# Kernel tuning notes

Hardware: AMD Instinct MI355X
Metric: run time of the kernel (lower is better)

## Reference

```python
import jax, jax.numpy as jnp
import numpy as np

B, T, C, H, N = 4, 4096, 2048, 32, 64
DMIX, DDEC = 32, 64
N_LAYER, LAYER_ID = 24, 12
GN_EPS = 1e-5 * 8.0 ** 2  # eps = 1e-5 * head_size_divisor**2


def setup_inputs() -> dict:
    key = jax.random.key(0)
    ks = jax.random.split(key, 24)
    r01 = LAYER_ID / (N_LAYER - 1)
    r1a0 = 1.0 - LAYER_ID / N_LAYER
    ddd = (np.arange(C, dtype=np.float32) / C).reshape(1, 1, C)
    maa = lambda p: jnp.asarray(1.0 - ddd ** p, dtype=jnp.float32)
    # decay speed schedule (canonical RWKV6, over channel dim)
    n = np.arange(C, dtype=np.float32)
    decay = (-6.0 + 5.0 * (n / (C - 1)) ** (0.7 + 1.3 * r01)).reshape(1, 1, C)
    # time_faaaa zigzag schedule
    m = np.arange(C, dtype=np.float32)
    zig = ((m + 1) % 3 - 1) * 0.1
    faaaa = (r01 * (1 - m / (C - 1)) + zig).reshape(H, N)
    s = 1.0 / np.sqrt(C)
    return {
        "x": jax.random.normal(ks[0], (B, T, C), jnp.float32),
        "shift_state": jax.random.normal(ks[1], (B, C), jnp.float32),
        "wkv_state": jnp.zeros((B, H, N, N), jnp.float32),
        "time_maa_x": maa(r1a0),
        "time_maa_w": maa(r1a0),
        "time_maa_k": maa(r1a0),
        "time_maa_v": jnp.asarray(1.0 - (ddd ** r1a0 + 0.3 * r01), jnp.float32),
        "time_maa_r": maa(0.5 * r1a0),
        "time_maa_g": maa(0.5 * r1a0),
        "time_maa_w1": jax.random.normal(ks[2], (C, 5 * DMIX), jnp.float32) * 0.01,
        "time_maa_w2": jax.random.uniform(ks[3], (5, DMIX, C), jnp.float32, -0.01, 0.01),
        "time_decay": jnp.asarray(decay, jnp.float32),
        "time_decay_w1": jax.random.normal(ks[4], (C, DDEC), jnp.float32) * 0.01,
        "time_decay_w2": jax.random.uniform(ks[5], (DDEC, C), jnp.float32, -0.01, 0.01),
        "time_faaaa": jnp.asarray(faaaa, jnp.float32),
        "Wr": jax.random.normal(ks[6], (C, C), jnp.float32) * s,
        "Wk": jax.random.normal(ks[7], (C, C), jnp.float32) * s,
        "Wv": jax.random.normal(ks[8], (C, C), jnp.float32) * s,
        "Wg": jax.random.normal(ks[9], (C, C), jnp.float32) * s,
        "Wo": jax.random.normal(ks[10], (C, C), jnp.float32) * s,
        "gn_weight": jnp.ones((C,), jnp.float32),
        "gn_bias": jnp.zeros((C,), jnp.float32),
    }


def reference(x, shift_state, wkv_state, time_maa_x, time_maa_w, time_maa_k,
              time_maa_v, time_maa_r, time_maa_g, time_maa_w1, time_maa_w2,
              time_decay, time_decay_w1, time_decay_w2, time_faaaa,
              Wr, Wk, Wv, Wg, Wo, gn_weight, gn_bias):
    b, t, c = x.shape
    # token shift: previous token (seeded by shift_state) minus current
    xx = jnp.concatenate([shift_state[:, None, :], x[:, :-1]], axis=1) - x
    lx = x[:, -1]
    # LoRA token-shift mixing
    xxx = x + xx * time_maa_x
    t5 = jnp.tanh(xxx @ time_maa_w1).reshape(b, t, 5, DMIX)
    mixes = jnp.einsum('btfd,fdc->fbtc', t5, time_maa_w2)
    mw, mk, mv, mr, mg = mixes
    xw = x + xx * (time_maa_w + mw)
    xk = x + xx * (time_maa_k + mk)
    xv = x + xx * (time_maa_v + mv)
    xr = x + xx * (time_maa_r + mr)
    xg = x + xx * (time_maa_g + mg)
    r = xr @ Wr
    k = xk @ Wk
    v = xv @ Wv
    g = jax.nn.silu(xg @ Wg)
    # data-dependent decay via LoRA; wkv6 uses log-decay -exp(w)
    w = time_decay + jnp.tanh(xw @ time_decay_w1) @ time_decay_w2
    glog = -jnp.exp(w)  # [b,t,c]
    to_heads = lambda z: z.reshape(b, t, H, N).transpose(1, 0, 2, 3)  # [t,b,h,n]
    rh, kh, vh, gh = to_heads(r), to_heads(k), to_heads(v), to_heads(glog)
    u = time_faaaa  # [H,N]

    def step(S, inp):
        r_t, k_t, v_t, g_t = inp  # each [b,h,n]
        kv = jnp.einsum('bhk,bhv->bhkv', k_t, v_t)
        o_t = jnp.einsum('bhk,bhkv->bhv', r_t, S + u[None, :, :, None] * kv)
        S = jnp.exp(g_t)[..., None] * S + kv
        return S, o_t

    state, o = jax.lax.scan(step, wkv_state, (rh, kh, vh, gh))
    o = o.transpose(1, 0, 2, 3).reshape(b, t, c)  # [b,t,c]
    # GroupNorm with H groups over channel dim
    og = o.reshape(b, t, H, N)
    mu = og.mean(-1, keepdims=True)
    var = og.var(-1, keepdims=True)
    on = (og - mu) * jax.lax.rsqrt(var + GN_EPS)
    on = on * gn_weight.reshape(H, N) + gn_bias.reshape(H, N)
    out = (on.reshape(b, t, c) * g) @ Wo
    return out, lx, state
```

## Files before the change

kernel.cpp:

```cpp
#include <hip/hip_runtime.h>
#include <hip/hip_bf16.h>
#include <stdint.h>

#define DEV __device__ __forceinline__

typedef __bf16 bf16x8 __attribute__((ext_vector_type(8)));
typedef float f32x4 __attribute__((ext_vector_type(4)));
typedef unsigned short u16x8 __attribute__((ext_vector_type(8)));

constexpr int kB = 4, kT = 4096, kC = 2048, kH = 32, kN = 64;
constexpr int kM = kB * kT;
constexpr int SEGN = 8, TSEG = kT / SEGN, CHN = TSEG / 64;

DEV float bfu2f(unsigned short u) {
  union { uint32_t i; float f; } x; x.i = ((uint32_t)u) << 16; return x.f;
}
DEV unsigned short f2bfu(float f) {
  union { float f; uint32_t i; } x; x.f = f;
  uint32_t r = x.i + 0x7FFFu + ((x.i >> 16) & 1u);
  return (unsigned short)(r >> 16);
}

DEV void gld16(const void* g, void* l) {
  __builtin_amdgcn_global_load_lds(
      (const __attribute__((address_space(1))) void*)g,
      (__attribute__((address_space(3))) void*)l, 16, 0, 0);
}

DEV int swzb(int row, int byteoff) { return (row << 7) + (byteoff ^ ((row & 7) << 4)); }
DEV int swz64(int row, int byteoff) { return (row << 6) + (byteoff ^ ((row & 3) << 4)); }

__global__ __launch_bounds__(256) void trans_bf16(
    const float* __restrict__ in, unsigned short* __restrict__ out, int R, int Cn) {
  __shared__ __attribute__((aligned(16))) unsigned short tile[64][65];
  const int t = threadIdx.x;
  const int r0 = blockIdx.y * 64, c0 = blockIdx.x * 64;
  const int lr = t >> 6, lc = t & 63;
#pragma unroll
  for (int i = 0; i < 16; i++) {
    int rr = lr + i * 4;
    int gr = r0 + rr, gc = c0 + lc;
    if (gr < R && gc < Cn) tile[rr][lc] = f2bfu(in[(size_t)gr * Cn + gc]);
  }
  __syncthreads();
#pragma unroll
  for (int i = 0; i < 16; i++) {
    int cc = lr + i * 4;
    int gc = c0 + cc, gr = r0 + lc;
    if (gc < Cn && gr < R) out[(size_t)gc * R + gr] = tile[lc][cc];
  }
}

__global__ __launch_bounds__(256) void prep_x2(
    const float* __restrict__ x, const float* __restrict__ shift,
    const float* __restrict__ maax,
    unsigned short* __restrict__ xxx, float* __restrict__ lx) {
  size_t i4 = ((size_t)blockIdx.x * 256 + threadIdx.x) * 4;
  int c = (int)(i4 & (kC - 1));
  size_t bt = i4 >> 11;
  int tt = (int)(bt & (kT - 1));
  int b = (int)(bt >> 12);
  float4 xv = *(const float4*)(x + i4);
  float4 pv = (tt == 0) ? *(const float4*)(shift + (size_t)b * kC + c)
                        : *(const float4*)(x + i4 - kC);
  float4 mx = *(const float4*)(maax + c);
  ushort4 o4;
  o4.x = f2bfu(xv.x + (pv.x - xv.x) * mx.x);
  o4.y = f2bfu(xv.y + (pv.y - xv.y) * mx.y);
  o4.z = f2bfu(xv.z + (pv.z - xv.z) * mx.z);
  o4.w = f2bfu(xv.w + (pv.w - xv.w) * mx.w);
  *(ushort4*)(xxx + i4) = o4;
  if (tt == kT - 1) *(float4*)(lx + (size_t)b * kC + c) = xv;
}

enum { E_F32 = 0, E_BF16 = 1, E_TANH = 2, E_SILU = 3 };

template <int BM, int BN, int EPI>
__global__ __launch_bounds__(256) void gemm_k(
    const unsigned short* __restrict__ A, const unsigned short* __restrict__ Bt,
    void* __restrict__ Cout, int M, int N, int K) {
  constexpr int WGM = (BM == 128 && BN == 128) ? 2 : (BM == 64 ? 2 : 4);
  constexpr int WGN = 4 / WGM;
  constexpr int WM = BM / WGM, WN = BN / WGN;
  constexpr int WR = WM / 16, WC = WN / 16;
  __shared__ __attribute__((aligned(16))) unsigned short As[BM * 32];
  __shared__ __attribute__((aligned(16))) unsigned short Bs[BN * 32];
  const int t = threadIdx.x, wid = t >> 6, l = t & 63;
  const int m0 = blockIdx.x * BM, n0 = blockIdx.y * BN;
  const int wm0 = (wid / WGN) * WM, wn0 = (wid % WGN) * WN;
  f32x4 acc[WR][WC];
#pragma unroll
  for (int i = 0; i < WR; i++)
#pragma unroll
    for (int j = 0; j < WC; j++) acc[i][j] = f32x4{0.f, 0.f, 0.f, 0.f};

  const int rowS = t >> 2, cbS = (t & 3) * 16;
  const char* Ab = (const char*)A;
  const char* Bb = (const char*)Bt;
  const int aoff = (wm0 + (l & 15)) * 32 + (l >> 4) * 8;
  const int boff = (wn0 + (l & 15)) * 32 + (l >> 4) * 8;

  for (int kt = 0; kt < K; kt += 32) {
#pragma unroll
    for (int ia = 0; ia < BM / 64; ia++)
      gld16(Ab + ((size_t)(m0 + ia * 64 + rowS) * K + kt) * 2 + cbS,
            (char*)As + ia * 4096 + wid * 1024);
    if constexpr (BN >= 64) {
#pragma unroll
      for (int ib = 0; ib < BN / 64; ib++)
        gld16(Bb + ((size_t)(n0 + ib * 64 + rowS) * K + kt) * 2 + cbS,
              (char*)Bs + ib * 4096 + wid * 1024);
    } else {
      if (t < BN * 4)
        gld16(Bb + ((size_t)(n0 + rowS) * K + kt) * 2 + cbS,
              (char*)Bs + wid * 1024);
    }
    __syncthreads();
    bf16x8 af[WR], bfv[WC];
#pragma unroll
    for (int mi = 0; mi < WR; mi++) af[mi] = *(const bf16x8*)(&As[aoff + mi * 512]);
#pragma unroll
    for (int ni = 0; ni < WC; ni++) bfv[ni] = *(const bf16x8*)(&Bs[boff + ni * 512]);
#pragma unroll
    for (int mi = 0; mi < WR; mi++)
#pragma unroll
      for (int ni = 0; ni < WC; ni++)
        acc[mi][ni] = __builtin_amdgcn_mfma_f32_16x16x32_bf16(af[mi], bfv[ni], acc[mi][ni], 0, 0, 0);
    __syncthreads();
  }

#pragma unroll
  for (int mi = 0; mi < WR; mi++) {
#pragma unroll
    for (int ni = 0; ni < WC; ni++) {
      int row = m0 + wm0 + mi * 16 + (l >> 4) * 4;
      int col = n0 + wn0 + ni * 16 + (l & 15);
#pragma unroll
      for (int j = 0; j < 4; j++) {
        float v = acc[mi][ni][j];
        size_t idx = (size_t)(row + j) * N + col;
        if constexpr (EPI == E_F32) ((float*)Cout)[idx] = v;
        else if constexpr (EPI == E_BF16) ((unsigned short*)Cout)[idx] = f2bfu(v);
        else if constexpr (EPI == E_TANH) ((unsigned short*)Cout)[idx] = f2bfu(tanhf(v));
        else if constexpr (EPI == E_SILU) ((unsigned short*)Cout)[idx] = f2bfu(v / (1.f + expf(-v)));
      }
    }
  }
}

template <int EPI>
__global__ __launch_bounds__(512, 2) void gemm256_k(
    const unsigned short* __restrict__ A, const unsigned short* __restrict__ Bt,
    void* __restrict__ Cout, int M, int N, int K) {
  extern __shared__ __attribute__((aligned(16))) char lds[];
  const int tid = threadIdx.x, wid = tid >> 6, l = tid & 63;
  const int fr = l & 15, fq = l >> 4;

  const int mtiles = M >> 8, ntiles = N >> 8;
  const int slab = mtiles >> 3;
  const int xcd = blockIdx.x & 7, loc = blockIdx.x >> 3;
  const int m0 = (xcd * slab + loc / ntiles) * 256;
  const int n0 = (loc % ntiles) * 256;

  const int wm = (wid >> 2) * 128, wn = (wid & 3) * 64;

  const int srow0 = tid >> 2;
  const int scb = ((tid & 3) * 16) ^ ((srow0 & 3) << 4);
  const char* pa2[2]; const char* pb2[2];
#pragma unroll
  for (int i = 0; i < 2; i++) {
    pa2[i] = (const char*)A + (size_t)(m0 + i * 128 + srow0) * K * 2 + scb;
    pb2[i] = (const char*)Bt + (size_t)(n0 + i * 128 + srow0) * K * 2 + scb;
  }

  const char* vA[8]; const char* vB[4];
#pragma unroll
  for (int mi = 0; mi < 8; mi++)
    vA[mi] = lds + swz64(wm + mi * 16 + fr, fq * 16);
#pragma unroll
  for (int ni = 0; ni < 4; ni++)
    vB[ni] = lds + 32768 + swz64(wn + ni * 16 + fr, fq * 16);

  f32x4 acc[8][4];
#pragma unroll
  for (int i = 0; i < 8; i++)
#pragma unroll
    for (int j = 0; j < 4; j++) acc[i][j] = f32x4{0.f, 0.f, 0.f, 0.f};

  auto STG = [&](int q, int s, int ktb) {
    const int d = q * 65536 + s * 16384 + wid * 1024;
    gld16(pa2[0] + ktb + s * 64, lds + d);
    gld16(pa2[1] + ktb + s * 64, lds + d + 8192);
    gld16(pb2[0] + ktb + s * 64, lds + 32768 + d);
    gld16(pb2[1] + ktb + s * 64, lds + 32768 + d + 8192);
  };

  auto PH = [&](int p, int s, bool doStage, int ktbNext, int vm) {
    if (vm)
      asm volatile("s_waitcnt vmcnt(4)" ::: "memory");
    else
      asm volatile("s_waitcnt vmcnt(0)" ::: "memory");
    __builtin_amdgcn_s_barrier();
    __builtin_amdgcn_sched_barrier(0);
    const int pb = p * 65536 + s * 16384;
    bf16x8 a[8], b[4];
#pragma unroll
    for (int mi = 0; mi < 8; mi++) a[mi] = *(const bf16x8*)(vA[mi] + pb);
#pragma unroll
    for (int ni = 0; ni < 4; ni++) b[ni] = *(const bf16x8*)(vB[ni] + pb);
    if (doStage) STG(p ^ 1, s, ktbNext);
    __builtin_amdgcn_sched_barrier(0);
    __builtin_amdgcn_s_setprio(1);
#pragma unroll
    for (int ni = 0; ni < 4; ni++)
#pragma unroll
      for (int mi = 0; mi < 8; mi++)
        acc[mi][ni] = __builtin_amdgcn_mfma_f32_16x16x32_bf16(a[mi], b[ni], acc[mi][ni], 0, 0, 0);
    __builtin_amdgcn_s_setprio(0);
  };

  const int KT = K >> 6;
  STG(0, 0, 0);
  STG(0, 1, 0);

  int T = 0;
  for (; T + 2 < KT; T += 2) {
    PH(0, 0, true, (T + 1) * 128, 4);
    PH(0, 1, true, (T + 1) * 128, 4);
    PH(1, 0, true, (T + 2) * 128, 4);
    PH(1, 1, true, (T + 2) * 128, 4);
  }
  PH(0, 0, true, (KT - 1) * 128, 4);
  PH(0, 1, true, (KT - 1) * 128, 4);
  PH(1, 0, false, 0, 4);
  PH(1, 1, false, 0, 0);

#pragma unroll
  for (int mi = 0; mi < 8; mi++)
#pragma unroll
    for (int ni = 0; ni < 4; ni++) {
      int row = m0 + wm + mi * 16 + fq * 4;
      int col = n0 + wn + ni * 16 + fr;
#pragma unroll
      for (int j = 0; j < 4; j++) {
        float v = acc[mi][ni][j];
        size_t idx = (size_t)(row + j) * N + col;
        if constexpr (EPI == E_F32) ((float*)Cout)[idx] = v;
        else if constexpr (EPI == E_BF16) ((unsigned short*)Cout)[idx] = f2bfu(v);
        else if constexpr (EPI == E_SILU) ((unsigned short*)Cout)[idx] = f2bfu(v / (1.f + expf(-v)));
      }
    }
}

__global__ __launch_bounds__(256) void mix5f_k(
    const unsigned short* __restrict__ t5, const unsigned short* __restrict__ w2t,
    const float* __restrict__ x, const float* __restrict__ shift,
    const float* __restrict__ maaw, const float* __restrict__ maak,
    const float* __restrict__ maav, const float* __restrict__ maar,
    const float* __restrict__ maag,
    unsigned short* __restrict__ xw, unsigned short* __restrict__ xk,
    unsigned short* __restrict__ xvo, unsigned short* __restrict__ xr,
    unsigned short* __restrict__ xg) {
  __shared__ __attribute__((aligned(16))) float tile[64][68];
  const int t = threadIdx.x, wid = t >> 6, l = t & 63;
  const int m0 = blockIdx.x * 64, n0 = blockIdx.y * 64;
  const int wm0 = (wid >> 1) * 32, wn0 = (wid & 1) * 32;
  const int fr = l & 15, fq = l >> 4;

  const unsigned short* pa0 = t5 + (size_t)(m0 + wm0 + fr) * 160 + fq * 8;
  const unsigned short* pa1 = t5 + (size_t)(m0 + wm0 + 16 + fr) * 160 + fq * 8;
  const unsigned short* pb0 = w2t + (size_t)(n0 + wn0 + fr) * 160 + fq * 8;
  const unsigned short* pb1 = w2t + (size_t)(n0 + wn0 + 16 + fr) * 160 + fq * 8;

  const int rrow = m0 + (t >> 2);
  const int c0 = (t & 3) * 16;
  const size_t base = (size_t)rrow * kC + n0 + c0;
  float xreg[16], dreg[16];
  {
    const int tt = rrow & (kT - 1);
    const float* pvp = (tt == 0) ? (shift + (size_t)(rrow >> 12) * kC + n0 + c0)
                                 : (x + base - kC);
#pragma unroll
    for (int q = 0; q < 4; q++) {
      float4 xv4 = *(const float4*)(x + base + q * 4);
      float4 pv4 = *(const float4*)(pvp + q * 4);
      xreg[q * 4 + 0] = xv4.x; dreg[q * 4 + 0] = pv4.x - xv4.x;
      xreg[q * 4 + 1] = xv4.y; dreg[q * 4 + 1] = pv4.y - xv4.y;
      xreg[q * 4 + 2] = xv4.z; dreg[q * 4 + 2] = pv4.z - xv4.z;
      xreg[q * 4 + 3] = xv4.w; dreg[q * 4 + 3] = pv4.w - xv4.w;
    }
  }

  unsigned short* outs[5] = { xw, xk, xvo, xr, xg };
  const float* maas[5] = { maaw, maak, maav, maar, maag };
#pragma unroll
  for (int f = 0; f < 5; f++) {
    bf16x8 a0 = *(const bf16x8*)(pa0 + f * 32);
    bf16x8 a1 = *(const bf16x8*)(pa1 + f * 32);
    bf16x8 b0 = *(const bf16x8*)(pb0 + f * 32);
    bf16x8 b1 = *(const bf16x8*)(pb1 + f * 32);
    f32x4 ac00 = __builtin_amdgcn_mfma_f32_16x16x32_bf16(a0, b0, f32x4{0.f, 0.f, 0.f, 0.f}, 0, 0, 0);
    f32x4 ac01 = __builtin_amdgcn_mfma_f32_16x16x32_bf16(a0, b1, f32x4{0.f, 0.f, 0.f, 0.f}, 0, 0, 0);
    f32x4 ac10 = __builtin_amdgcn_mfma_f32_16x16x32_bf16(a1, b0, f32x4{0.f, 0.f, 0.f, 0.f}, 0, 0, 0);
    f32x4 ac11 = __builtin_amdgcn_mfma_f32_16x16x32_bf16(a1, b1, f32x4{0.f, 0.f, 0.f, 0.f}, 0, 0, 0);
    __syncthreads();
#pragma unroll
    for (int j = 0; j < 4; j++) {
      tile[wm0 + fq * 4 + j][wn0 + fr]            = ac00[j];
      tile[wm0 + fq * 4 + j][wn0 + 16 + fr]       = ac01[j];
      tile[wm0 + 16 + fq * 4 + j][wn0 + fr]       = ac10[j];
      tile[wm0 + 16 + fq * 4 + j][wn0 + 16 + fr]  = ac11[j];
    }
    __syncthreads();
    const float* mp = maas[f] + n0 + c0;
    u16x8 o0, o1;
#pragma unroll
    for (int q = 0; q < 4; q++) {
      f32x4 m4 = *(const f32x4*)&tile[t >> 2][c0 + q * 4];
      float4 ma4 = *(const float4*)(mp + q * 4);
      float mv[4] = { ma4.x, ma4.y, ma4.z, ma4.w };
#pragma unroll
      for (int e = 0; e < 4; e++) {
        int i = q * 4 + e;
        unsigned short r = f2bfu(xreg[i] + dreg[i] * (mv[e] + m4[e]));
        if (i < 8) o0[i] = r; else o1[i - 8] = r;
      }
    }
    *(u16x8*)(outs[f] + base) = o0;
    *(u16x8*)(outs[f] + base + 8) = o1;
  }
}

__global__ __launch_bounds__(256) void wkv_local_k(
    const unsigned short* __restrict__ kb, const unsigned short* __restrict__ vb,
    const unsigned short* __restrict__ dtmp, const unsigned short* __restrict__ td2t,
    const float* __restrict__ tdec,
    float* __restrict__ Lbuf, float* __restrict__ Dseg) {
  const int bid = blockIdx.x;
  const int bh = bid >> 3, seg = bid & 7;
  const int h = bh & 31, b = bh >> 5;
  const int tid = threadIdx.x, w = tid >> 6, l = tid & 63;
  __shared__ __attribute__((aligned(16))) char arena[32768];
  char* KQks = arena;
  char* Vt   = arena + 8192;
  float* EdB = (float*)arena;
  char* TdB  = arena + 16384;
  char* DtA  = arena + 24576;
  __shared__ float segp[4][64];
  __shared__ float DLs[64];
  __shared__ float tdf[64];

  const int fr = l & 15, fq = l >> 4;
  f32x4 Sreg[4];
#pragma unroll
  for (int ni = 0; ni < 4; ni++) Sreg[ni] = f32x4{0.f, 0.f, 0.f, 0.f};

  {
    int r1 = tid >> 3, r2 = 32 + r1;
    int cb1 = ((tid & 7) * 16) ^ ((r1 & 7) << 4);
    int cb2 = ((tid & 7) * 16) ^ ((r2 & 7) << 4);
    gld16((const char*)td2t + (size_t)(h * 64 + r1) * 128 + cb1, TdB + w * 1024);
    gld16((const char*)td2t + (size_t)(h * 64 + r2) * 128 + cb2, TdB + 4096 + w * 1024);
    if (tid < 64) tdf[tid] = tdec[h * 64 + tid];
  }

  float dtot = 1.f;
  float kv[16], vv[16];
  {
    size_t g = ((size_t)b * kT + seg * TSEG + w * 16) * kC + h * 64 + l;
#pragma unroll
    for (int i = 0; i < 16; i++) {
      kv[i] = bfu2f(kb[g]); vv[i] = bfu2f(vb[g]);
      g += kC;
    }
  }

  for (int ch = 0; ch < CHN; ++ch) {
    const size_t gt0 = (size_t)b * kT + seg * TSEG + ch * 64;
    {
      int r1 = tid >> 3, r2 = 32 + r1;
      int cb1 = ((tid & 7) * 16) ^ ((r1 & 7) << 4);
      int cb2 = ((tid & 7) * 16) ^ ((r2 & 7) << 4);
      gld16((const char*)dtmp + (gt0 + r1) * 128 + cb1, DtA + w * 1024);
      gld16((const char*)dtmp + (gt0 + r2) * 128 + cb2, DtA + 4096 + w * 1024);
    }
    __syncthreads();

    f32x4 dacc[4];
    {
      bf16x8 af0 = *(const bf16x8*)(DtA + swzb(w * 16 + fr, fq * 16));
      bf16x8 af1 = *(const bf16x8*)(DtA + swzb(w * 16 + fr, fq * 16 + 64));
#pragma unroll
      for (int nj = 0; nj < 4; nj++) {
        bf16x8 b0 = *(const bf16x8*)(TdB + swzb(nj * 16 + fr, fq * 16));
        bf16x8 b1 = *(const bf16x8*)(TdB + swzb(nj * 16 + fr, fq * 16 + 64));
        dacc[nj] = __builtin_amdgcn_mfma_f32_16x16x32_bf16(af0, b0, f32x4{0.f, 0.f, 0.f, 0.f}, 0, 0, 0);
        dacc[nj] = __builtin_amdgcn_mfma_f32_16x16x32_bf16(af1, b1, dacc[nj], 0, 0, 0);
      }
    }
#pragma unroll
    for (int nj = 0; nj < 4; nj++) {
      float tv = tdf[nj * 16 + fr];
#pragma unroll
      for (int j = 0; j < 4; j++)
        EdB[(w * 16 + fq * 4 + j) * 64 + nj * 16 + fr] = expf(-expf(dacc[nj][j] + tv));
    }
    float dvv[16];
    float p = 1.f;
#pragma unroll
    for (int i = 0; i < 16; i++) {
      float d = EdB[(w * 16 + i) * 64 + l];
      dvv[i] = d; p *= d;
    }
    segp[w][l] = p;
    __syncthreads();

    float pre = 1.f;
    if (w > 0) pre *= segp[0][l];
    if (w > 1) pre *= segp[1][l];
    if (w > 2) pre *= segp[2][l];
    if (w == 3) DLs[l] = pre * p;

    unsigned short kqrow[16], vtrow[16];
    float run = pre;
#pragma unroll
    for (int i = 0; i < 16; i++) {
      run *= dvv[i];
      kqrow[i] = f2bfu(kv[i] / run);
      vtrow[i] = f2bfu(vv[i]);
    }
    {
      u16x8 q0, q1, v0, v1;
#pragma unroll
      for (int j = 0; j < 8; j++) { q0[j] = kqrow[j]; q1[j] = kqrow[j + 8]; v0[j] = vtrow[j]; v1[j] = vtrow[j + 8]; }
      *(u16x8*)(KQks + swzb(l, w * 32)) = q0;
      *(u16x8*)(KQks + swzb(l, w * 32 + 16)) = q1;
      *(u16x8*)(Vt + swzb(l, w * 32)) = v0;
      *(u16x8*)(Vt + swzb(l, w * 32 + 16)) = v1;
    }
    if (ch < CHN - 1) {
      size_t g = ((size_t)b * kT + seg * TSEG + (ch + 1) * 64 + w * 16) * kC + h * 64 + l;
#pragma unroll
      for (int i = 0; i < 16; i++) {
        kv[i] = bfu2f(kb[g]); vv[i] = bfu2f(vb[g]);
        g += kC;
      }
    }
    __syncthreads();

    bf16x8 kA0 = *(const bf16x8*)(KQks + swzb(w * 16 + fr, fq * 16));
    bf16x8 kA1 = *(const bf16x8*)(KQks + swzb(w * 16 + fr, fq * 16 + 64));
    f32x4 kvacc[4];
#pragma unroll
    for (int ni = 0; ni < 4; ni++) {
      bf16x8 bv0 = *(const bf16x8*)(Vt + swzb(ni * 16 + fr, fq * 16));
      bf16x8 bv1 = *(const bf16x8*)(Vt + swzb(ni * 16 + fr, fq * 16 + 64));
      kvacc[ni] = __builtin_amdgcn_mfma_f32_16x16x32_bf16(kA0, bv0, f32x4{0.f, 0.f, 0.f, 0.f}, 0, 0, 0);
      kvacc[ni] = __builtin_amdgcn_mfma_f32_16x16x32_bf16(kA1, bv1, kvacc[ni], 0, 0, 0);
    }
    float dlj[4];
#pragma unroll
    for (int j = 0; j < 4; j++) dlj[j] = DLs[w * 16 + fq * 4 + j];
#pragma unroll
    for (int ni = 0; ni < 4; ni++)
#pragma unroll
      for (int j = 0; j < 4; j++)
        Sreg[ni][j] = (Sreg[ni][j] + kvacc[ni][j]) * dlj[j];
    dtot *= DLs[l];
  }

  float* Lp = Lbuf + (size_t)bid * 4096;
#pragma unroll
  for (int ni = 0; ni < 4; ni++)
#pragma unroll
    for (int j = 0; j < 4; j++)
      Lp[(size_t)(w * 16 + fq * 4 + j) * 64 + ni * 16 + fr] = Sreg[ni][j];
  if (w == 0) Dseg[(size_t)bid * 64 + l] = dtot;
}

__global__ __launch_bounds__(256) void wkv_combine_k(
    const float* __restrict__ s0, const float* __restrict__ Dseg,
    float* __restrict__ Lbuf, float* __restrict__ sOut) {
  const int bh = blockIdx.x, tid = threadIdx.x;
  const int k = tid >> 2, v0 = (tid & 3) * 16;
  float4 s[4];
  const float* sp = s0 + (size_t)bh * 4096 + (size_t)k * 64 + v0;
#pragma unroll
  for (int q = 0; q < 4; q++) s[q] = ((const float4*)sp)[q];
  for (int seg = 0; seg < SEGN; ++seg) {
    size_t idx = (size_t)bh * SEGN + seg;
    float d = Dseg[idx * 64 + k];
    float* Lp = Lbuf + idx * 4096 + (size_t)k * 64 + v0;
#pragma unroll
    for (int q = 0; q < 4; q++) {
      float4 lq = ((float4*)Lp)[q];
      ((float4*)Lp)[q] = s[q];
      s[q].x = d * s[q].x + lq.x; s[q].y = d * s[q].y + lq.y;
      s[q].z = d * s[q].z + lq.z; s[q].w = d * s[q].w + lq.w;
    }
  }
  float* op = sOut + (size_t)bh * 4096 + (size_t)k * 64 + v0;
#pragma unroll
  for (int q = 0; q < 4; q++) ((float4*)op)[q] = s[q];
}

__global__ __launch_bounds__(256) void wkv_seg_k(
    const unsigned short* __restrict__ rb, const unsigned short* __restrict__ kb,
    const unsigned short* __restrict__ vb,
    const unsigned short* __restrict__ dtmp, const unsigned short* __restrict__ td2t,
    const float* __restrict__ tdec,
    const float* __restrict__ uf, const float* __restrict__ Sini,
    unsigned short* __restrict__ o) {
  const int bid = blockIdx.x;
  const int bh = bid >> 3, seg = bid & 7;
  const int h = bh & 31, b = bh >> 5;
  const int tid = threadIdx.x, w = tid >> 6, l = tid & 63;
  __shared__ __attribute__((aligned(16))) char arena[65536];
  char* RQ   = arena;
  char* KQsk = arena + 8192;
  char* KQks = arena + 16384;
  char* Vt   = arena + 24576;
  char* Pl   = arena + 32768;
  char* S0T  = arena + 40960;
  char* RU   = arena + 49152;
  char* Ksk  = arena + 57344;
  float* EdB = (float*)arena;
  char* DtA  = RU;
  char* TdB  = Ksk;
  __shared__ float segp[4][64];
  __shared__ float DLs[64];
  __shared__ float tdf[64];

  const float uu = uf[h * 64 + l];
  const int fr = l & 15, fq = l >> 4;
  if (tid < 64) tdf[tid] = tdec[h * 64 + tid];

  f32x4 Sreg[4];
#pragma unroll
  for (int ni = 0; ni < 4; ni++)
#pragma unroll
    for (int j = 0; j < 4; j++) {
      int kk2 = w * 16 + fq * 4 + j, vv2 = ni * 16 + fr;
      float sv = Sini[(size_t)bid * 4096 + (size_t)kk2 * 64 + vv2];
      Sreg[ni][j] = sv;
      *(unsigned short*)(S0T + swzb(vv2, kk2 * 2)) = f2bfu(sv);
    }
  __syncthreads();

  float rv[16], kv[16], vv[16];
  {
    size_t g = ((size_t)b * kT + seg * TSEG + w * 16) * kC + h * 64 + l;
#pragma unroll
    for (int i = 0; i < 16; i++) {
      rv[i] = bfu2f(rb[g]); kv[i] = bfu2f(kb[g]); vv[i] = bfu2f(vb[g]);
      g += kC;
    }
  }

  const int r1s = tid >> 3, r2s = 32 + r1s;
  const int cb1 = ((tid & 7) * 16) ^ ((r1s & 7) << 4);
  const int cb2 = ((tid & 7) * 16) ^ ((r2s & 7) << 4);

  for (int ch = 0; ch < CHN; ++ch) {
    const size_t gt0 = (size_t)b * kT + seg * TSEG + ch * 64;
    gld16((const char*)dtmp + (gt0 + r1s) * 128 + cb1, DtA + w * 1024);
    gld16((const char*)dtmp + (gt0 + r2s) * 128 + cb2, DtA + 4096 + w * 1024);
    gld16((const char*)td2t + (size_t)(h * 64 + r1s) * 128 + cb1, TdB + w * 1024);
    gld16((const char*)td2t + (size_t)(h * 64 + r2s) * 128 + cb2, TdB + 4096 + w * 1024);
    __syncthreads();

    f32x4 dacc[4];
    {
      bf16x8 af0 = *(const bf16x8*)(DtA + swzb(w * 16 + fr, fq * 16));
      bf16x8 af1 = *(const bf16x8*)(DtA + swzb(w * 16 + fr, fq * 16 + 64));
#pragma unroll
      for (int nj = 0; nj < 4; nj++) {
        bf16x8 b0 = *(const bf16x8*)(TdB + swzb(nj * 16 + fr, fq * 16));
        bf16x8 b1 = *(const bf16x8*)(TdB + swzb(nj * 16 + fr, fq * 16 + 64));
        dacc[nj] = __builtin_amdgcn_mfma_f32_16x16x32_bf16(af0, b0, f32x4{0.f, 0.f, 0.f, 0.f}, 0, 0, 0);
        dacc[nj] = __builtin_amdgcn_mfma_f32_16x16x32_bf16(af1, b1, dacc[nj], 0, 0, 0);
      }
    }
#pragma unroll
    for (int nj = 0; nj < 4; nj++) {
      float tv = tdf[nj * 16 + fr];
#pragma unroll
      for (int j = 0; j < 4; j++)
        EdB[(w * 16 + fq * 4 + j) * 64 + nj * 16 + fr] = expf(-expf(dacc[nj][j] + tv));
    }
    float dv[16];
    float p = 1.f;
#pragma unroll
    for (int i = 0; i < 16; i++) {
      dv[i] = EdB[(w * 16 + i) * 64 + l];
      p *= dv[i];
    }
    segp[w][l] = p;
    __syncthreads();

    float pre = 1.f;
    if (w > 0) pre *= segp[0][l];
    if (w > 1) pre *= segp[1][l];
    if (w > 2) pre *= segp[2][l];
    if (w == 3) DLs[l] = pre * p;

    unsigned short kqrow[16], vtrow[16];
    float run = pre;
#pragma unroll
    for (int i = 0; i < 16; i++) {
      int t = w * 16 + i;
      float rq = rv[i] * run;
      run *= dv[i];
      float kq = kv[i] / run;
      *(unsigned short*)(RQ + swzb(t, l * 2)) = f2bfu(rq);
      *(unsigned short*)(RU + swzb(t, l * 2)) = f2bfu(rv[i] * uu);
      *(unsigned short*)(Ksk + swzb(t, l * 2)) = f2bfu(kv[i]);
      unsigned short kqu = f2bfu(kq);
      *(unsigned short*)(KQsk + swzb(t, l * 2)) = kqu;
      kqrow[i] = kqu;
      vtrow[i] = f2bfu(vv[i]);
    }
    {
      u16x8 q0, q1, v0, v1;
#pragma unroll
      for (int j = 0; j < 8; j++) { q0[j] = kqrow[j]; q1[j] = kqrow[j + 8]; v0[j] = vtrow[j]; v1[j] = vtrow[j + 8]; }
      *(u16x8*)(KQks + swzb(l, w * 32)) = q0;
      *(u16x8*)(KQks + swzb(l, w * 32 + 16)) = q1;
      *(u16x8*)(Vt + swzb(l, w * 32)) = v0;
      *(u16x8*)(Vt + swzb(l, w * 32 + 16)) = v1;
    }

    if (ch < CHN - 1) {
      size_t g = ((size_t)b * kT + seg * TSEG + (ch + 1) * 64 + w * 16) * kC + h * 64 + l;
#pragma unroll
      for (int i = 0; i < 16; i++) {
        rv[i] = bfu2f(rb[g]); kv[i] = bfu2f(kb[g]); vv[i] = bfu2f(vb[g]);
        g += kC;
      }
    }
    __syncthreads();

    bf16x8 a0 = *(const bf16x8*)(RQ + swzb(w * 16 + fr, fq * 16));
    bf16x8 a1 = *(const bf16x8*)(RQ + swzb(w * 16 + fr, fq * 16 + 64));
    f32x4 pacc[4];
#pragma unroll
    for (int ni = 0; ni < 4; ni++) {
      bf16x8 b0 = *(const bf16x8*)(KQsk + swzb(ni * 16 + fr, fq * 16));
      bf16x8 b1 = *(const bf16x8*)(KQsk + swzb(ni * 16 + fr, fq * 16 + 64));
      pacc[ni] = __builtin_amdgcn_mfma_f32_16x16x32_bf16(a0, b0, f32x4{0.f, 0.f, 0.f, 0.f}, 0, 0, 0);
      pacc[ni] = __builtin_amdgcn_mfma_f32_16x16x32_bf16(a1, b1, pacc[ni], 0, 0, 0);
    }
    f32x4 dacc2;
    {
      bf16x8 ru0 = *(const bf16x8*)(RU + swzb(w * 16 + fr, fq * 16));
      bf16x8 ru1 = *(const bf16x8*)(RU + swzb(w * 16 + fr, fq * 16 + 64));
      bf16x8 kb0 = *(const bf16x8*)(Ksk + swzb(w * 16 + fr, fq * 16));
      bf16x8 kb1 = *(const bf16x8*)(Ksk + swzb(w * 16 + fr, fq * 16 + 64));
      dacc2 = __builtin_amdgcn_mfma_f32_16x16x32_bf16(ru0, kb0, f32x4{0.f, 0.f, 0.f, 0.f}, 0, 0, 0);
      dacc2 = __builtin_amdgcn_mfma_f32_16x16x32_bf16(ru1, kb1, dacc2, 0, 0, 0);
    }
    float dg[4];
#pragma unroll
    for (int j = 0; j < 4; j++) dg[j] = __shfl(dacc2[j], fq * 20 + j, 64);
#pragma unroll
    for (int ni = 0; ni < 4; ni++)
#pragma unroll
      for (int j = 0; j < 4; j++) {
        int row = w * 16 + fq * 4 + j, col = ni * 16 + fr;
        float pv = pacc[ni][j];
        pv = (col < row) ? pv : ((col == row) ? dg[j] : 0.f);
        *(unsigned short*)(Pl + swzb(row, col * 2)) = f2bfu(pv);
      }
    __syncthreads();

    bf16x8 pA0 = *(const bf16x8*)(Pl + swzb(w * 16 + fr, fq * 16));
    bf16x8 pA1 = *(const bf16x8*)(Pl + swzb(w * 16 + fr, fq * 16 + 64));
    bf16x8 kA0 = *(const bf16x8*)(KQks + swzb(w * 16 + fr, fq * 16));
    bf16x8 kA1 = *(const bf16x8*)(KQks + swzb(w * 16 + fr, fq * 16 + 64));
    f32x4 oacc[4], kvacc[4];
#pragma unroll
    for (int ni = 0; ni < 4; ni++) {
      bf16x8 bv0 = *(const bf16x8*)(Vt + swzb(ni * 16 + fr, fq * 16));
      bf16x8 bv1 = *(const bf16x8*)(Vt + swzb(ni * 16 + fr, fq * 16 + 64));
      bf16x8 bs0 = *(const bf16x8*)(S0T + swzb(ni * 16 + fr, fq * 16));
      bf16x8 bs1 = *(const bf16x8*)(S0T + swzb(ni * 16 + fr, fq * 16 + 64));
      oacc[ni] = __builtin_amdgcn_mfma_f32_16x16x32_bf16(pA0, bv0, f32x4{0.f, 0.f, 0.f, 0.f}, 0, 0, 0);
      oacc[ni] = __builtin_amdgcn_mfma_f32_16x16x32_bf16(pA1, bv1, oacc[ni], 0, 0, 0);
      oacc[ni] = __builtin_amdgcn_mfma_f32_16x16x32_bf16(a0, bs0, oacc[ni], 0, 0, 0);
      oacc[ni] = __builtin_amdgcn_mfma_f32_16x16x32_bf16(a1, bs1, oacc[ni], 0, 0, 0);
      kvacc[ni] = __builtin_amdgcn_mfma_f32_16x16x32_bf16(kA0, bv0, f32x4{0.f, 0.f, 0.f, 0.f}, 0, 0, 0);
      kvacc[ni] = __builtin_amdgcn_mfma_f32_16x16x32_bf16(kA1, bv1, kvacc[ni], 0, 0, 0);
    }
    size_t obase = gt0 * kC + h * 64;
#pragma unroll
    for (int ni = 0; ni < 4; ni++)
#pragma unroll
      for (int j = 0; j < 4; j++)
        o[obase + (size_t)(w * 16 + fq * 4 + j) * kC + ni * 16 + fr] = f2bfu(oacc[ni][j]);
    __syncthreads();

    float dlj[4];
#pragma unroll
    for (int j = 0; j < 4; j++) dlj[j] = DLs[w * 16 + fq * 4 + j];
#pragma unroll
    for (int ni = 0; ni < 4; ni++)
#pragma unroll
      for (int j = 0; j < 4; j++) {
        int kk2 = w * 16 + fq * 4 + j, vv2 = ni * 16 + fr;
        float sn = (Sreg[ni][j] + kvacc[ni][j]) * dlj[j];
        Sreg[ni][j] = sn;
        *(unsigned short*)(S0T + swzb(vv2, kk2 * 2)) = f2bfu(sn);
      }
  }
}

__global__ __launch_bounds__(256) void gn_k(
    const unsigned short* __restrict__ o, const unsigned short* __restrict__ gb,
    const float* __restrict__ gnw, const float* __restrict__ gnb,
    unsigned short* __restrict__ y) {
  int gi = blockIdx.x * 4 + (threadIdx.x >> 6);
  int j = threadIdx.x & 63;
  int bt = gi >> 5, h = gi & 31;
  size_t idx = (size_t)bt * kC + h * 64 + j;
  float val = bfu2f(o[idx]);
  float s = val, s2 = val * val;
#pragma unroll
  for (int m = 1; m < 64; m <<= 1) {
    s += __shfl_xor(s, m, 64);
    s2 += __shfl_xor(s2, m, 64);
  }
  float mu = s * 0.015625f;
  float var = s2 * 0.015625f - mu * mu;
  float rs = rsqrtf(var + 6.4e-4f);
  float on = (val - mu) * rs * gnw[h * 64 + j] + gnb[h * 64 + j];
  y[idx] = f2bfu(on * bfu2f(gb[idx]));
}

constexpr size_t SZW     = (size_t)2048 * 2048 * 2;
constexpr size_t OFF_WRT = 0;
constexpr size_t OFF_WKT = 1 * SZW;
constexpr size_t OFF_WVT = 2 * SZW;
constexpr size_t OFF_WGT = 3 * SZW;
constexpr size_t OFF_WOT = 4 * SZW;
constexpr size_t OFF_W1T = 5 * SZW;
constexpr size_t OFF_W2T = OFF_W1T + (size_t)160 * 2048 * 2;
constexpr size_t OFF_TD1 = OFF_W2T + (size_t)2048 * 160 * 2;
constexpr size_t OFF_TD2 = OFF_TD1 + (size_t)64 * 2048 * 2;
constexpr size_t OFF_T5  = OFF_TD2 + (size_t)2048 * 64 * 2;
constexpr size_t OFF_DT  = OFF_T5 + (size_t)kM * 160 * 2;
constexpr size_t OFF_XG  = OFF_DT + (size_t)kM * 64 * 2;
constexpr size_t OFF_X   = OFF_XG + (size_t)kM * kC * 4;
constexpr size_t OFF_R   = OFF_X + (size_t)kM * kC * 2;
constexpr size_t OFF_K   = OFF_R + (size_t)kM * kC * 2;
constexpr size_t OFF_V   = OFF_K + (size_t)kM * kC * 2;
constexpr size_t OFF_L   = OFF_WRT;

extern "C" void kernel_launch(void* const* d_in, const int* in_sizes, int n_in,
                              void* d_out, int out_size, void* d_ws, size_t ws_size,
                              hipStream_t stream) {
  const float* x     = (const float*)d_in[0];
  const float* shift = (const float*)d_in[1];
  const float* s0    = (const float*)d_in[2];
  const float* maax  = (const float*)d_in[3];
  const float* maaw  = (const float*)d_in[4];
  const float* maak  = (const float*)d_in[5];
  const float* maav  = (const float*)d_in[6];
  const float* maar  = (const float*)d_in[7];
  const float* maag  = (const float*)d_in[8];
  const float* w1    = (const float*)d_in[9];
  const float* w2    = (const float*)d_in[10];
  const float* tdec  = (const float*)d_in[11];
  const float* tdw1  = (const float*)d_in[12];
  const float* tdw2  = (const float*)d_in[13];
  const float* faaaa = (const float*)d_in[14];
  const float* Wr    = (const float*)d_in[15];
  const float* Wk    = (const float*)d_in[16];
  const float* Wv    = (const float*)d_in[17];
  const float* Wg    = (const float*)d_in[18];
  const float* Wo    = (const float*)d_in[19];
  const float* gnw   = (const float*)d_in[20];
  const float* gnb   = (const float*)d_in[21];

  char* ws = (char*)d_ws;
  unsigned short* Wrt  = (unsigned short*)(ws + OFF_WRT);
  unsigned short* Wkt  = (unsigned short*)(ws + OFF_WKT);
  unsigned short* Wvt  = (unsigned short*)(ws + OFF_WVT);
  unsigned short* Wgt  = (unsigned short*)(ws + OFF_WGT);
  unsigned short* Wot  = (unsigned short*)(ws + OFF_WOT);
  unsigned short* w1t  = (unsigned short*)(ws + OFF_W1T);
  unsigned short* w2t  = (unsigned short*)(ws + OFF_W2T);
  unsigned short* td1t = (unsigned short*)(ws + OFF_TD1);
  unsigned short* td2t = (unsigned short*)(ws + OFF_TD2);
  unsigned short* t5   = (unsigned short*)(ws + OFF_T5);
  unsigned short* dtmp = (unsigned short*)(ws + OFF_DT);
  unsigned short* xg   = (unsigned short*)(ws + OFF_XG);
  unsigned short* obuf = (unsigned short*)(ws + OFF_XG);
  unsigned short* ybuf = (unsigned short*)(ws + OFF_XG) + (size_t)kM * kC;
  unsigned short* bufX = (unsigned short*)(ws + OFF_X);
  unsigned short* bufR = (unsigned short*)(ws + OFF_R);
  unsigned short* bufK = (unsigned short*)(ws + OFF_K);
  unsigned short* bufV = (unsigned short*)(ws + OFF_V);
  float*          Lbuf = (float*)(ws + OFF_L);
  float*          DsegP= (float*)(ws + OFF_TD1);

  float* outp  = (float*)d_out;
  float* lx    = outp + (size_t)kM * kC;
  float* stOut = lx + (size_t)kB * kC;

  dim3 blk(256);

  trans_bf16<<<dim3(32, 32), blk, 0, stream>>>(Wr, Wrt, 2048, 2048);
  trans_bf16<<<dim3(32, 32), blk, 0, stream>>>(Wk, Wkt, 2048, 2048);
  trans_bf16<<<dim3(32, 32), blk, 0, stream>>>(Wv, Wvt, 2048, 2048);
  trans_bf16<<<dim3(32, 32), blk, 0, stream>>>(Wg, Wgt, 2048, 2048);
  trans_bf16<<<dim3(32, 32), blk, 0, stream>>>(Wo, Wot, 2048, 2048);
  trans_bf16<<<dim3(3, 32), blk, 0, stream>>>(w1, w1t, 2048, 160);
  trans_bf16<<<dim3(1, 32), blk, 0, stream>>>(tdw1, td1t, 2048, 64);
  trans_bf16<<<dim3(32, 1), blk, 0, stream>>>(tdw2, td2t, 64, 2048);
  trans_bf16<<<dim3(32, 3), blk, 0, stream>>>(w2, w2t, 160, 2048);

  prep_x2<<<dim3(kM * kC / 4 / 256), blk, 0, stream>>>(x, shift, maax, bufX, lx);

  gemm_k<128, 32, E_TANH><<<dim3(kM / 128, 5), blk, 0, stream>>>(bufX, w1t, t5, kM, 160, 2048);

  dim3 mgrid(kM / 64, kC / 64);
  constexpr int G256 = (kM / 256) * (kC / 256);
  constexpr size_t LDS256 = 131072;

  mix5f_k<<<mgrid, blk, 0, stream>>>(t5, w2t, x, shift, maaw, maak, maav, maar, maag,
                                     bufX, bufV, bufR, bufK, xg);
  gemm_k<64, 64, E_TANH><<<dim3(kM / 64, 1), blk, 0, stream>>>(bufX, td1t, dtmp, kM, 64, 2048);

  gemm256_k<E_BF16><<<dim3(G256), dim3(512), LDS256, stream>>>(bufV, Wkt, bufX, kM, 2048, 2048);
  gemm256_k<E_BF16><<<dim3(G256), dim3(512), LDS256, stream>>>(bufR, Wvt, bufV, kM, 2048, 2048);
  gemm256_k<E_BF16><<<dim3(G256), dim3(512), LDS256, stream>>>(bufK, Wrt, bufR, kM, 2048, 2048);
  gemm256_k<E_SILU><<<dim3(G256), dim3(512), LDS256, stream>>>(xg, Wgt, bufK, kM, 2048, 2048);

  wkv_local_k<<<dim3(kB * kH * SEGN), blk, 0, stream>>>(bufX, bufV, dtmp, td2t, tdec,
                                                        Lbuf, DsegP);
  wkv_combine_k<<<dim3(kB * kH), blk, 0, stream>>>(s0, DsegP, Lbuf, stOut);
  wkv_seg_k<<<dim3(kB * kH * SEGN), blk, 0, stream>>>(bufR, bufX, bufV, dtmp, td2t, tdec,
                                                      faaaa, Lbuf, obuf);

  gn_k<<<dim3(kM * kH / 4), blk, 0, stream>>>(obuf, bufK, gnw, gnb, ybuf);

  gemm256_k<E_F32><<<dim3(G256), dim3(512), LDS256, stream>>>(ybuf, Wot, outp, kM, 2048, 2048);
}
```

Before: 1.436 ms.

## Restructure 256x256 GEMM main loop into 4-phase ping-pong with 128B swizzle

Rewrites the bf16 256x256-tile GEMM mainloop to use full 64-wide K tiles with a 128-byte XOR swizzle. Each K tile is split into four phases: each phase loads A fragments for two M subtiles, and B fragments are reused across phases. Global-to-LDS staging of the next tile is split between phases 0 and 1 (A then B). Barriers bracket each MFMA cluster, launch bounds drop to one block per CU, and a single vmcnt(0) wait per tile replaces the old per-phase waits. The aim is better overlap of LDS reads with MFMA and fewer redundant LDS loads, at the cost of more barriers and lower occupancy.

```diff
diff --git a/kernel.cpp b/kernel.cpp
--- a/kernel.cpp
+++ b/kernel.cpp
@@ -28,7 +28,6 @@
 }
 
 DEV int swzb(int row, int byteoff) { return (row << 7) + (byteoff ^ ((row & 7) << 4)); }
-DEV int swz64(int row, int byteoff) { return (row << 6) + (byteoff ^ ((row & 3) << 4)); }
 
 __global__ __launch_bounds__(256) void trans_bf16(
     const float* __restrict__ in, unsigned short* __restrict__ out, int R, int Cn) {
@@ -148,13 +147,63 @@
   }
 }
 
+#define GPH(PP, QQ, SKIND, KTB)                                                        \
+  do {                                                                                 \
+    const int aB_ = (PP) * 65536 + wr * 16384;                                         \
+    const int bB_ = 32768 + (PP) * 65536 + bh * 16384;                                 \
+    if ((QQ) == 0) {                                                                   \
+      _Pragma("unroll")                                                                \
+      for (int ni = 0; ni < 4; ni++) {                                                 \
+        bfr[ni][0] = *(const bf16x8*)(lds + bB_ + bRow[ni] + bOffK0);                  \
+        bfr[ni][1] = *(const bf16x8*)(lds + bB_ + bRow[ni] + bOffK1);                  \
+      }                                                                                \
+    }                                                                                  \
+    bf16x8 a0k0_ = *(const bf16x8*)(lds + aB_ + (2 * (QQ)) * 2048 + aOffK0);           \
+    bf16x8 a0k1_ = *(const bf16x8*)(lds + aB_ + (2 * (QQ)) * 2048 + aOffK1);           \
+    bf16x8 a1k0_ = *(const bf16x8*)(lds + aB_ + (2 * (QQ) + 1) * 2048 + aOffK0);       \
+    bf16x8 a1k1_ = *(const bf16x8*)(lds + aB_ + (2 * (QQ) + 1) * 2048 + aOffK1);       \
+    if ((SKIND) == 1) {                                                                \
+      const int d_ = ((PP) ^ 1) * 65536;                                               \
+      gld16(pA0 + (KTB), lds + d_ + tid * 16);                                         \
+      gld16(pA0 + (KTB) + (size_t)64 * kC * 2, lds + d_ + 8192 + tid * 16);            \
+      gld16(pA1 + (KTB), lds + d_ + 16384 + tid * 16);                                 \
+      gld16(pA1 + (KTB) + (size_t)64 * kC * 2, lds + d_ + 24576 + tid * 16);           \
+    } else if ((SKIND) == 2) {                                                         \
+      const int d_ = 32768 + (((PP) ^ 1) * 65536);                                     \
+      gld16(pB0 + (KTB), lds + d_ + tid * 16);                                         \
+      gld16(pB0 + (KTB) + (size_t)64 * kC * 2, lds + d_ + 8192 + tid * 16);            \
+      gld16(pB1 + (KTB), lds + d_ + 16384 + tid * 16);                                 \
+      gld16(pB1 + (KTB) + (size_t)64 * kC * 2, lds + d_ + 24576 + tid * 16);           \
+    }                                                                                  \
+    __builtin_amdgcn_s_barrier();                                                      \
+    asm volatile("s_waitcnt lgkmcnt(0)" ::: "memory");                                 \
+    __builtin_amdgcn_sched_barrier(0);                                                 \
+    __builtin_amdgcn_s_setprio(1);                                                     \
+    _Pragma("unroll")                                                                  \
+    for (int ni = 0; ni < 4; ni++) {                                                   \
+      acc[2 * (QQ)][ni] = __builtin_amdgcn_mfma_f32_16x16x32_bf16(a0k0_, bfr[ni][0], acc[2 * (QQ)][ni], 0, 0, 0);         \
+      acc[2 * (QQ) + 1][ni] = __builtin_amdgcn_mfma_f32_16x16x32_bf16(a1k0_, bfr[ni][0], acc[2 * (QQ) + 1][ni], 0, 0, 0); \
+      acc[2 * (QQ)][ni] = __builtin_amdgcn_mfma_f32_16x16x32_bf16(a0k1_, bfr[ni][1], acc[2 * (QQ)][ni], 0, 0, 0);         \
+      acc[2 * (QQ) + 1][ni] = __builtin_amdgcn_mfma_f32_16x16x32_bf16(a1k1_, bfr[ni][1], acc[2 * (QQ) + 1][ni], 0, 0, 0); \
+    }                                                                                  \
+    __builtin_amdgcn_s_setprio(0);                                                     \
+    if ((QQ) == 3) {                                                                   \
+      asm volatile("s_waitcnt vmcnt(0)" ::: "memory");                                 \
+      __builtin_amdgcn_sched_barrier(0);                                               \
+    }                                                                                  \
+    __builtin_amdgcn_s_barrier();                                                      \
+    __builtin_amdgcn_sched_barrier(0);                                                 \
+  } while (0)
+
 template <int EPI>
-__global__ __launch_bounds__(512, 2) void gemm256_k(
+__global__ __launch_bounds__(512, 1) void gemm256_k(
     const unsigned short* __restrict__ A, const unsigned short* __restrict__ Bt,
     void* __restrict__ Cout, int M, int N, int K) {
   extern __shared__ __attribute__((aligned(16))) char lds[];
   const int tid = threadIdx.x, wid = tid >> 6, l = tid & 63;
   const int fr = l & 15, fq = l >> 4;
+  const int wr = wid >> 2, wc = wid & 3;
+  const int bh = wc >> 1;
 
   const int mtiles = M >> 8, ntiles = N >> 8;
   const int slab = mtiles >> 3;
@@ -162,85 +211,59 @@
   const int m0 = (xcd * slab + loc / ntiles) * 256;
   const int n0 = (loc % ntiles) * 256;
 
-  const int wm = (wid >> 2) * 128, wn = (wid & 3) * 64;
-
-  const int srow0 = tid >> 2;
-  const int scb = ((tid & 3) * 16) ^ ((srow0 & 3) << 4);
-  const char* pa2[2]; const char* pb2[2];
-#pragma unroll
-  for (int i = 0; i < 2; i++) {
-    pa2[i] = (const char*)A + (size_t)(m0 + i * 128 + srow0) * K * 2 + scb;
-    pb2[i] = (const char*)Bt + (size_t)(n0 + i * 128 + srow0) * K * 2 + scb;
-  }
-
-  const char* vA[8]; const char* vB[4];
-#pragma unroll
-  for (int mi = 0; mi < 8; mi++)
-    vA[mi] = lds + swz64(wm + mi * 16 + fr, fq * 16);
-#pragma unroll
-  for (int ni = 0; ni < 4; ni++)
-    vB[ni] = lds + 32768 + swz64(wn + ni * 16 + fr, fq * 16);
+  const int sr = tid >> 3;
+  const int scb = ((tid & 7) * 16) ^ ((sr & 7) << 4);
+  const char* pA0 = (const char*)A + (size_t)(m0 + sr) * K * 2 + scb;
+  const char* pA1 = (const char*)A + (size_t)(m0 + 128 + sr) * K * 2 + scb;
+  const char* pB0 = (const char*)Bt + (size_t)(n0 + sr) * K * 2 + scb;
+  const char* pB1 = (const char*)Bt + (size_t)(n0 + 128 + sr) * K * 2 + scb;
+
+  const int xorv = (fr & 7) << 4;
+  const int aOffK0 = fr * 128 + ((fq * 16) ^ xorv);
+  const int aOffK1 = fr * 128 + ((64 + fq * 16) ^ xorv);
+  const int bOffK0 = aOffK0, bOffK1 = aOffK1;
+  int bRow[4];
+#pragma unroll
+  for (int ni = 0; ni < 4; ni++) bRow[ni] = ((wc & 1) * 64 + ni * 16) * 128;
 
   f32x4 acc[8][4];
 #pragma unroll
   for (int i = 0; i < 8; i++)
 #pragma unroll
     for (int j = 0; j < 4; j++) acc[i][j] = f32x4{0.f, 0.f, 0.f, 0.f};
-
-  auto STG = [&](int q, int s, int ktb) {
-    const int d = q * 65536 + s * 16384 + wid * 1024;
-    gld16(pa2[0] + ktb + s * 64, lds + d);
-    gld16(pa2[1] + ktb + s * 64, lds + d + 8192);
-    gld16(pb2[0] + ktb + s * 64, lds + 32768 + d);
-    gld16(pb2[1] + ktb + s * 64, lds + 32768 + d + 8192);
-  };
-
-  auto PH = [&](int p, int s, bool doStage, int ktbNext, int vm) {
-    if (vm)
-      asm volatile("s_waitcnt vmcnt(4)" ::: "memory");
-    else
-      asm volatile("s_waitcnt vmcnt(0)" ::: "memory");
+  bf16x8 bfr[4][2];
+
+  const int KT = K >> 6;
+  {
+    gld16(pA0, lds + tid * 16);
+    gld16(pA0 + (size_t)64 * kC * 2, lds + 8192 + tid * 16);
+    gld16(pA1, lds + 16384 + tid * 16);
+    gld16(pA1 + (size_t)64 * kC * 2, lds + 24576 + tid * 16);
+    gld16(pB0, lds + 32768 + tid * 16);
+    gld16(pB0 + (size_t)64 * kC * 2, lds + 32768 + 8192 + tid * 16);
+    gld16(pB1, lds + 32768 + 16384 + tid * 16);
+    gld16(pB1 + (size_t)64 * kC * 2, lds + 32768 + 24576 + tid * 16);
+    asm volatile("s_waitcnt vmcnt(0)" ::: "memory");
     __builtin_amdgcn_s_barrier();
     __builtin_amdgcn_sched_barrier(0);
-    const int pb = p * 65536 + s * 16384;
-    bf16x8 a[8], b[4];
-#pragma unroll
-    for (int mi = 0; mi < 8; mi++) a[mi] = *(const bf16x8*)(vA[mi] + pb);
-#pragma unroll
-    for (int ni = 0; ni < 4; ni++) b[ni] = *(const bf16x8*)(vB[ni] + pb);
-    if (doStage) STG(p ^ 1, s, ktbNext);
-    __builtin_amdgcn_sched_barrier(0);
-    __builtin_amdgcn_s_setprio(1);
-#pragma unroll
-    for (int ni = 0; ni < 4; ni++)
-#pragma unroll
-      for (int mi = 0; mi < 8; mi++)
-        acc[mi][ni] = __builtin_amdgcn_mfma_f32_16x16x32_bf16(a[mi], b[ni], acc[mi][ni], 0, 0, 0);
-    __builtin_amdgcn_s_setprio(0);
-  };
-
-  const int KT = K >> 6;
-  STG(0, 0, 0);
-  STG(0, 1, 0);
-
-  int T = 0;
-  for (; T + 2 < KT; T += 2) {
-    PH(0, 0, true, (T + 1) * 128, 4);
-    PH(0, 1, true, (T + 1) * 128, 4);
-    PH(1, 0, true, (T + 2) * 128, 4);
-    PH(1, 1, true, (T + 2) * 128, 4);
-  }
-  PH(0, 0, true, (KT - 1) * 128, 4);
-  PH(0, 1, true, (KT - 1) * 128, 4);
-  PH(1, 0, false, 0, 4);
-  PH(1, 1, false, 0, 0);
+  }
+
+  for (int T = 0; T < KT; ++T) {
+    const int p = T & 1;
+    const int st = (T + 1 < KT) ? 1 : 0;
+    const int ktb = (T + 1) * 128;
+    GPH(p, 0, st ? 1 : 0, ktb);
+    GPH(p, 1, st ? 2 : 0, ktb);
+    GPH(p, 2, 0, 0);
+    GPH(p, 3, 0, 0);
+  }
 
 #pragma unroll
   for (int mi = 0; mi < 8; mi++)
 #pragma unroll
     for (int ni = 0; ni < 4; ni++) {
-      int row = m0 + wm + mi * 16 + fq * 4;
-      int col = n0 + wn + ni * 16 + fr;
+      int row = m0 + wr * 128 + mi * 16 + fq * 4;
+      int col = n0 + wc * 64 + ni * 16 + fr;
 #pragma unroll
       for (int j = 0; j < 4; j++) {
         float v = acc[mi][ni][j];
```

Measured after the change: 1.430 ms. About the same (-0.4%).
